# Optimization experiments

Measured on AMD Instinct MI355X. Metric: run time of the kernel, lower is better.

## Reference

```python
import jax, jax.numpy as jnp
import numpy as np

H, R, B, T = 512, 4, 16, 4096

def _glorot(key, shape):
    return jax.random.uniform(key, shape, minval=-1.0, maxval=1.0) * jnp.sqrt(2.0 / sum(shape))

def setup_inputs() -> dict:
    key = jax.random.key(0)
    k1, k2, k3, k4, k5 = jax.random.split(key, 5)
    return {
        "x_seq": jax.random.normal(k5, (B, T, H), dtype=jnp.float32),
        "a_diag": _glorot(k1, (H,)).astype(jnp.float32),
        "p_vec": _glorot(k2, (H, R)).astype(jnp.float32),
        "q_vec": _glorot(k3, (H, R)).astype(jnp.float32),
        "b_mat": _glorot(k4, (H, H)).astype(jnp.float32),
    }

def reference(x_seq, a_diag, p_vec, q_vec, b_mat):
    # A = diag(a_diag) + P Q^T  (DPLR structure, materialized as in the source)
    A = jnp.diag(a_diag) + p_vec @ q_vec.T            # [H, H]
    # Precompute B @ x_t for all timesteps/batches: bx[b,t,k] = sum_h b_mat[k,h] x[b,t,h]
    bx = jnp.einsum("bth,kh->btk", x_seq, b_mat)      # [B, T, H]
    h0 = jnp.zeros((x_seq.shape[0], a_diag.shape[0]), dtype=x_seq.dtype)  # [B, H]

    def step(h, bx_t):
        # h_{t} = A h_{t-1} + B x_t, batched: (h @ A^T)
        h = h @ A.T + bx_t
        return h, h

    _, h_seq = jax.lax.scan(step, h0, jnp.swapaxes(bx, 0, 1))  # [T, B, H]
    return jnp.swapaxes(h_seq, 0, 1)                            # [B, T, H]
```

## Files before the change

kernel.cpp:

```cpp
#include <hip/hip_runtime.h>
#include <hip/hip_bf16.h>

#define H 512
#define RNK 4
#define BATCH 16
#define TT 4096
#define MTOT (BATCH * TT)

#define BM 128
#define BN 128
#define BK 64

#define NCHUNK 128
#define JWARM 32

#define LDK 72

typedef __attribute__((ext_vector_type(8))) short bf16x8;
typedef __attribute__((ext_vector_type(4))) float f32x4;

__device__ inline unsigned short f2bf(float f) {
    unsigned u = __float_as_uint(f);
    u += 0x7FFFu + ((u >> 16) & 1u);
    return (unsigned short)(u >> 16);
}
__device__ inline float bflo(unsigned w) { return __uint_as_float(w << 16); }
__device__ inline float bfhi(unsigned w) { return __uint_as_float(w & 0xFFFF0000u); }
__device__ inline float rfl(float x) {
    return __uint_as_float(__builtin_amdgcn_readfirstlane(__float_as_uint(x)));
}

__global__ __launch_bounds__(256) void convert_kernel(
    const float* __restrict__ src, unsigned short* __restrict__ dst, int n4)
{
    int i = blockIdx.x * blockDim.x + threadIdx.x;
    const int stride = gridDim.x * blockDim.x;
    for (; i < n4; i += stride) {
        float4 v = ((const float4*)src)[i];
        ushort4 o = { f2bf(v.x), f2bf(v.y), f2bf(v.z), f2bf(v.w) };
        ((ushort4*)dst)[i] = o;
    }
}

__global__ __launch_bounds__(256) void gemm_bt_kernel(
    const unsigned short* __restrict__ A,
    const unsigned short* __restrict__ Bm,
    unsigned short* __restrict__ C)
{
    __shared__ unsigned short As[BM * BK];
    __shared__ unsigned short Bs[BN * BK];
    const int tid  = threadIdx.x;
    const int lane = tid & 63;
    const int wave = tid >> 6;
    const int wm = (wave >> 1) * 64;
    const int wn = (wave & 1) * 64;
    const size_t m0 = (size_t)blockIdx.x * BM;
    const int n0 = blockIdx.y * BN;
    const int r  = lane & 15;
    const int qd = lane >> 4;

    f32x4 acc[4][4];
    #pragma unroll
    for (int i = 0; i < 4; ++i)
        #pragma unroll
        for (int j = 0; j < 4; ++j)
            acc[i][j] = (f32x4){0.f, 0.f, 0.f, 0.f};

    for (int k0 = 0; k0 < H; k0 += BK) {
        #pragma unroll
        for (int s = 0; s < 4; ++s) {
            const int seg = wave * 4 + s;
            const int off = seg * 1024 + lane * 16;
            const int row = off >> 7;
            const int inrow = off & 127;
            const char* ga = (const char*)(A + (m0 + row) * H + k0) + inrow;
            const char* gb = (const char*)(Bm + (size_t)(n0 + row) * H + k0) + inrow;
            __builtin_amdgcn_global_load_lds(
                (const __attribute__((address_space(1))) unsigned int*)ga,
                (__attribute__((address_space(3))) unsigned int*)&As[seg * 512], 16, 0, 0);
            __builtin_amdgcn_global_load_lds(
                (const __attribute__((address_space(1))) unsigned int*)gb,
                (__attribute__((address_space(3))) unsigned int*)&Bs[seg * 512], 16, 0, 0);
        }
        __syncthreads();
        #pragma unroll
        for (int kk = 0; kk < BK; kk += 32) {
            bf16x8 af[4], bfr[4];
            #pragma unroll
            for (int i = 0; i < 4; ++i)
                af[i] = *(const bf16x8*)&As[(wm + i * 16 + r) * BK + kk + qd * 8];
            #pragma unroll
            for (int j = 0; j < 4; ++j)
                bfr[j] = *(const bf16x8*)&Bs[(wn + j * 16 + r) * BK + kk + qd * 8];
            #pragma unroll
            for (int i = 0; i < 4; ++i)
                #pragma unroll
                for (int j = 0; j < 4; ++j)
                    acc[i][j] = __builtin_amdgcn_mfma_f32_16x16x32_bf16(
                        af[i], bfr[j], acc[i][j], 0, 0, 0);
        }
        __syncthreads();
    }
    #pragma unroll
    for (int i = 0; i < 4; ++i)
        #pragma unroll
        for (int j = 0; j < 4; ++j)
            #pragma unroll
            for (int e = 0; e < 4; ++e) {
                const size_t m = m0 + wm + i * 16 + qd * 4 + e;
                const int n = n0 + wn + j * 16 + r;
                C[m * H + n] = f2bf(acc[i][j][e]);
            }
}

__global__ __launch_bounds__(64) void scan_bf_kernel(
    const unsigned short* __restrict__ bx, float* __restrict__ out,
    const float* __restrict__ a_diag, const float* __restrict__ p_vec,
    const float* __restrict__ q_vec, int nchunk, int warm_max)
{
    const int lane = threadIdx.x;
    const int c = blockIdx.x;
    const int b = blockIdx.y;
    const int L = TT / nchunk;
    const int d0 = lane * 8;

    float ak[8], g[8];
    float4 pk[8], qk[8];
    #pragma unroll
    for (int j = 0; j < 8; ++j) {
        ak[j] = a_diag[d0 + j];
        pk[j] = *(const float4*)(p_vec + (d0 + j) * RNK);
        qk[j] = *(const float4*)(q_vec + (d0 + j) * RNK);
        g[j] = 0.f;
    }

    float Gx[3][4][4];
    {
        float part[3][16];
        #pragma unroll
        for (int k = 0; k < 3; ++k)
            #pragma unroll
            for (int v = 0; v < 16; ++v) part[k][v] = 0.f;
        #pragma unroll
        for (int d = 0; d < 8; ++d) {
            const float a1 = ak[d], a2 = a1 * a1;
            const float qr[4] = {qk[d].x, qk[d].y, qk[d].z, qk[d].w};
            const float pc[4] = {pk[d].x, pk[d].y, pk[d].z, pk[d].w};
            #pragma unroll
            for (int r = 0; r < 4; ++r)
                #pragma unroll
                for (int cc = 0; cc < 4; ++cc) {
                    const float qp = qr[r] * pc[cc];
                    part[0][r * 4 + cc] += qp;
                    part[1][r * 4 + cc] += qp * a1;
                    part[2][r * 4 + cc] += qp * a2;
                }
        }
        #pragma unroll
        for (int off = 32; off > 0; off >>= 1)
            #pragma unroll
            for (int k = 0; k < 3; ++k)
                #pragma unroll
                for (int v = 0; v < 16; ++v)
                    part[k][v] += __shfl_xor(part[k][v], off);
        #pragma unroll
        for (int k = 0; k < 3; ++k)
            #pragma unroll
            for (int r = 0; r < 4; ++r)
                #pragma unroll
                for (int cc = 0; cc < 4; ++cc)
                    Gx[k][r][cc] = rfl(part[k][r * 4 + cc]);
    }

    const int warm  = (c == 0) ? 0 : warm_max;
    const int steps = warm + L;
    const int nb    = steps >> 2;
    const int tstart = c * L - warm;
    const unsigned short* src = bx + (size_t)b * TT * H + d0;
    float* dst = out + (size_t)b * TT * H + d0;

    uint4 ring[4];
    #pragma unroll
    for (int j = 0; j < 4; ++j)
        ring[j] = *(const uint4*)(src + (size_t)(tstart + j) * H);

    for (int blk = 0; blk < nb; ++blk) {
        const int i0 = blk * 4;
        float yp[4][4];
        float gs[4][8];

        #pragma unroll
        for (int j = 0; j < 4; ++j) {
            float y0 = 0.f, y1 = 0.f, y2 = 0.f, y3 = 0.f;
            #pragma unroll
            for (int d = 0; d < 8; ++d) {
                y0 += qk[d].x * g[d]; y1 += qk[d].y * g[d];
                y2 += qk[d].z * g[d]; y3 += qk[d].w * g[d];
            }
            yp[j][0] = y0; yp[j][1] = y1; yp[j][2] = y2; yp[j][3] = y3;

            const uint4 cur = ring[j];
            int iload = i0 + 4 + j;
            if (iload > steps - 1) iload = steps - 1;
            ring[j] = *(const uint4*)(src + (size_t)(tstart + iload) * H);

            float u[8];
            u[0] = bflo(cur.x); u[1] = bfhi(cur.x);
            u[2] = bflo(cur.y); u[3] = bfhi(cur.y);
            u[4] = bflo(cur.z); u[5] = bfhi(cur.z);
            u[6] = bflo(cur.w); u[7] = bfhi(cur.w);
            #pragma unroll
            for (int d = 0; d < 8; ++d) { g[d] = ak[d] * g[d] + u[d]; gs[j][d] = g[d]; }
        }

        #pragma unroll
        for (int off = 32; off > 0; off >>= 1)
            #pragma unroll
            for (int j = 0; j < 4; ++j)
                #pragma unroll
                for (int r = 0; r < 4; ++r)
                    yp[j][r] += __shfl_xor(yp[j][r], off);

        float sv[4][4];
        #pragma unroll
        for (int r = 0; r < 4; ++r) sv[0][r] = yp[0][r];
        #pragma unroll
        for (int r = 0; r < 4; ++r) {
            float t = yp[1][r];
            #pragma unroll
            for (int cc = 0; cc < 4; ++cc) t += Gx[0][r][cc] * sv[0][cc];
            sv[1][r] = t;
        }
        #pragma unroll
        for (int r = 0; r < 4; ++r) {
            float t = yp[2][r];
            #pragma unroll
            for (int cc = 0; cc < 4; ++cc) t += Gx[1][r][cc] * sv[0][cc];
            #pragma unroll
            for (int cc = 0; cc < 4; ++cc) t += Gx[0][r][cc] * sv[1][cc];
            sv[2][r] = t;
        }
        #pragma unroll
        for (int r = 0; r < 4; ++r) {
            float t = yp[3][r];
            #pragma unroll
            for (int cc = 0; cc < 4; ++cc) t += Gx[2][r][cc] * sv[0][cc];
            #pragma unroll
            for (int cc = 0; cc < 4; ++cc) t += Gx[1][r][cc] * sv[1][cc];
            #pragma unroll
            for (int cc = 0; cc < 4; ++cc) t += Gx[0][r][cc] * sv[2][cc];
            sv[3][r] = t;
        }

        const bool dostore = (i0 >= warm);
        float e[8];
        #pragma unroll
        for (int d = 0; d < 8; ++d) e[d] = 0.f;
        #pragma unroll
        for (int j = 0; j < 4; ++j) {
            #pragma unroll
            for (int d = 0; d < 8; ++d) {
                const float ps = pk[d].x * sv[j][0] + pk[d].y * sv[j][1]
                               + pk[d].z * sv[j][2] + pk[d].w * sv[j][3];
                e[d] = ak[d] * e[d] + ps;
            }
            if (dostore) {
                float* dd = dst + (size_t)(tstart + i0 + j) * H;
                *(float4*)dd       = (float4){gs[j][0] + e[0], gs[j][1] + e[1],
                                              gs[j][2] + e[2], gs[j][3] + e[3]};
                *(float4*)(dd + 4) = (float4){gs[j][4] + e[4], gs[j][5] + e[5],
                                              gs[j][6] + e[6], gs[j][7] + e[7]};
            }
        }
        #pragma unroll
        for (int d = 0; d < 8; ++d) g[d] = gs[3][d] + e[d];
    }
}

__global__ __launch_bounds__(256) void gemm_fused_kernel(
    const float* __restrict__ X, const float* __restrict__ W, float* __restrict__ bx)
{
    __shared__ unsigned short As[BM * LDK];
    __shared__ unsigned short Bs[BN * LDK];
    const int tid  = threadIdx.x;
    const int lane = tid & 63;
    const int wave = tid >> 6;
    const int wm = (wave >> 1) * 64;
    const int wn = (wave & 1) * 64;
    const size_t mbase = (size_t)blockIdx.x * BM;
    const int nbase = blockIdx.y * BN;
    const float* Xb = X + mbase * H;
    const float* Wb = W + (size_t)nbase * H;
    f32x4 acc[4][4];
    #pragma unroll
    for (int i = 0; i < 4; ++i)
        #pragma unroll
        for (int j = 0; j < 4; ++j)
            acc[i][j] = (f32x4){0.f, 0.f, 0.f, 0.f};
    const int r  = lane & 15;
    const int qd = lane >> 4;
    for (int k0 = 0; k0 < H; k0 += BK) {
        #pragma unroll
        for (int i = 0; i < 8; ++i) {
            int idx = tid + i * 256;
            int row = idx >> 4;
            int c4  = (idx & 15) * 4;
            float4 va = *(const float4*)(Xb + (size_t)row * H + k0 + c4);
            float4 vb = *(const float4*)(Wb + (size_t)row * H + k0 + c4);
            ushort4 wa = { f2bf(va.x), f2bf(va.y), f2bf(va.z), f2bf(va.w) };
            ushort4 wb = { f2bf(vb.x), f2bf(vb.y), f2bf(vb.z), f2bf(vb.w) };
            *(ushort4*)&As[row * LDK + c4] = wa;
            *(ushort4*)&Bs[row * LDK + c4] = wb;
        }
        __syncthreads();
        #pragma unroll
        for (int kk = 0; kk < BK; kk += 32) {
            bf16x8 af[4], bfr[4];
            #pragma unroll
            for (int i = 0; i < 4; ++i)
                af[i] = *(const bf16x8*)&As[(wm + i * 16 + r) * LDK + kk + qd * 8];
            #pragma unroll
            for (int j = 0; j < 4; ++j)
                bfr[j] = *(const bf16x8*)&Bs[(wn + j * 16 + r) * LDK + kk + qd * 8];
            #pragma unroll
            for (int i = 0; i < 4; ++i)
                #pragma unroll
                for (int j = 0; j < 4; ++j)
                    acc[i][j] = __builtin_amdgcn_mfma_f32_16x16x32_bf16(
                        af[i], bfr[j], acc[i][j], 0, 0, 0);
        }
        __syncthreads();
    }
    #pragma unroll
    for (int i = 0; i < 4; ++i)
        #pragma unroll
        for (int j = 0; j < 4; ++j)
            #pragma unroll
            for (int e = 0; e < 4; ++e) {
                int m = wm + i * 16 + qd * 4 + e;
                int n = wn + j * 16 + r;
                bx[(mbase + m) * H + nbase + n] = acc[i][j][e];
            }
}

__global__ __launch_bounds__(64) void scan_f32_kernel(
    const float* __restrict__ bx, float* __restrict__ out,
    const float* __restrict__ a_diag, const float* __restrict__ p_vec,
    const float* __restrict__ q_vec)
{
    const int lane = threadIdx.x;
    const int b = blockIdx.y;
    const int d0 = lane * 8;
    float ak[8], hk[8];
    float4 pk[8], qk[8];
    #pragma unroll
    for (int j = 0; j < 8; ++j) {
        ak[j] = a_diag[d0 + j];
        pk[j] = *(const float4*)(p_vec + (d0 + j) * RNK);
        qk[j] = *(const float4*)(q_vec + (d0 + j) * RNK);
        hk[j] = 0.f;
    }
    const float* src = bx + (size_t)b * TT * H + d0;
    float* dst = out + (size_t)b * TT * H + d0;
    for (int i = 0; i < TT; ++i) {
        const float* sp = src + (size_t)i * H;
        float4 va = *(const float4*)sp, vb = *(const float4*)(sp + 4);
        float u[8] = {va.x, va.y, va.z, va.w, vb.x, vb.y, vb.z, vb.w};
        float s0 = 0.f, s1 = 0.f, s2 = 0.f, s3 = 0.f;
        #pragma unroll
        for (int j = 0; j < 8; ++j) {
            s0 += qk[j].x * hk[j]; s1 += qk[j].y * hk[j];
            s2 += qk[j].z * hk[j]; s3 += qk[j].w * hk[j];
        }
        #pragma unroll
        for (int off = 32; off > 0; off >>= 1) {
            s0 += __shfl_xor(s0, off); s1 += __shfl_xor(s1, off);
            s2 += __shfl_xor(s2, off); s3 += __shfl_xor(s3, off);
        }
        #pragma unroll
        for (int j = 0; j < 8; ++j)
            hk[j] = ak[j] * hk[j] + (pk[j].x * s0 + pk[j].y * s1 + pk[j].z * s2 + pk[j].w * s3) + u[j];
        float* d = dst + (size_t)i * H;
        *(float4*)d = (float4){hk[0], hk[1], hk[2], hk[3]};
        *(float4*)(d + 4) = (float4){hk[4], hk[5], hk[6], hk[7]};
    }
}

extern "C" void kernel_launch(void* const* d_in, const int* in_sizes, int n_in,
                              void* d_out, int out_size, void* d_ws, size_t ws_size,
                              hipStream_t stream) {
    (void)in_sizes; (void)n_in; (void)out_size;
    const float* x = (const float*)d_in[0];
    const float* a = (const float*)d_in[1];
    const float* p = (const float*)d_in[2];
    const float* q = (const float*)d_in[3];
    const float* w = (const float*)d_in[4];
    float* out = (float*)d_out;

    const size_t nx    = (size_t)MTOT * H;
    const size_t xbf_b = nx * 2;
    const size_t wbf_b = (size_t)H * H * 2;
    const size_t bxb_b = nx * 2;

    unsigned short *xbf = nullptr, *wbf = nullptr, *bxbf = nullptr;
    if (ws_size >= xbf_b + wbf_b + bxb_b) {
        xbf  = (unsigned short*)d_ws;
        wbf  = xbf + nx;
        bxbf = wbf + (size_t)H * H;
    } else if (ws_size >= bxb_b) {
        xbf  = (unsigned short*)d_out;
        wbf  = xbf + nx;
        bxbf = (unsigned short*)d_ws;
    }

    if (bxbf != nullptr) {
        convert_kernel<<<8192, 256, 0, stream>>>(x, xbf, (int)(nx / 4));
        convert_kernel<<<256, 256, 0, stream>>>(w, wbf, (int)(H * H / 4));
        dim3 g1(MTOT / BM, H / BN), b1(256);
        gemm_bt_kernel<<<g1, b1, 0, stream>>>(xbf, wbf, bxbf);
        dim3 g2(NCHUNK, BATCH), b2(64);
        scan_bf_kernel<<<g2, b2, 0, stream>>>(bxbf, out, a, p, q, NCHUNK, JWARM);
    } else {
        dim3 g1(MTOT / BM, H / BN), b1(256);
        gemm_fused_kernel<<<g1, b1, 0, stream>>>(x, w, out);
        dim3 g2(1, BATCH), b2(64);
        scan_f32_kernel<<<g2, b2, 0, stream>>>(out, out, a, p, q);
    }
}
```

Measured before the change: 342.5 us.

## Fuse fp32-to-bf16 conversion into GEMM loads and remap tile order

Drops the separate conversion kernels for x and W. The GEMM now reads fp32 directly, converts to bf16 in registers, and stores into padded LDS tiles (stride 72) to cut bank conflicts. A 1D grid with a swizzled block-to-tile mapping groups the four N-tiles of each M-block across XCDs. This removes a full write and reread of the bf16 copy of x. In exchange it loses the async global_load_lds path and doubles global read bytes per GEMM tile, since fp32 is read and every M-tile of x is loaded four times.

```diff
diff --git a/kernel.cpp b/kernel.cpp
--- a/kernel.cpp
+++ b/kernel.cpp
@@ -30,57 +30,43 @@
     return __uint_as_float(__builtin_amdgcn_readfirstlane(__float_as_uint(x)));
 }
 
-__global__ __launch_bounds__(256) void convert_kernel(
-    const float* __restrict__ src, unsigned short* __restrict__ dst, int n4)
+__global__ __launch_bounds__(256) void gemm_fused_bt_kernel(
+    const float* __restrict__ X, const float* __restrict__ W, unsigned short* __restrict__ C)
 {
-    int i = blockIdx.x * blockDim.x + threadIdx.x;
-    const int stride = gridDim.x * blockDim.x;
-    for (; i < n4; i += stride) {
-        float4 v = ((const float4*)src)[i];
-        ushort4 o = { f2bf(v.x), f2bf(v.y), f2bf(v.z), f2bf(v.w) };
-        ((ushort4*)dst)[i] = o;
-    }
-}
-
-__global__ __launch_bounds__(256) void gemm_bt_kernel(
-    const unsigned short* __restrict__ A,
-    const unsigned short* __restrict__ Bm,
-    unsigned short* __restrict__ C)
-{
-    __shared__ unsigned short As[BM * BK];
-    __shared__ unsigned short Bs[BN * BK];
+    __shared__ unsigned short As[BM * LDK];
+    __shared__ unsigned short Bs[BN * LDK];
+    const int l = blockIdx.x;
+    const int t = (l & 7) * ((MTOT / BM) * (H / BN) / 8) + (l >> 3);
+    const size_t mbase = (size_t)(t >> 2) * BM;
+    const int nbase = (t & 3) * BN;
+
     const int tid  = threadIdx.x;
     const int lane = tid & 63;
     const int wave = tid >> 6;
     const int wm = (wave >> 1) * 64;
     const int wn = (wave & 1) * 64;
-    const size_t m0 = (size_t)blockIdx.x * BM;
-    const int n0 = blockIdx.y * BN;
+    const float* Xb = X + mbase * H;
+    const float* Wb = W + (size_t)nbase * H;
+    f32x4 acc[4][4];
+    #pragma unroll
+    for (int i = 0; i < 4; ++i)
+        #pragma unroll
+        for (int j = 0; j < 4; ++j)
+            acc[i][j] = (f32x4){0.f, 0.f, 0.f, 0.f};
     const int r  = lane & 15;
     const int qd = lane >> 4;
-
-    f32x4 acc[4][4];
-    #pragma unroll
-    for (int i = 0; i < 4; ++i)
-        #pragma unroll
-        for (int j = 0; j < 4; ++j)
-            acc[i][j] = (f32x4){0.f, 0.f, 0.f, 0.f};
-
     for (int k0 = 0; k0 < H; k0 += BK) {
         #pragma unroll
-        for (int s = 0; s < 4; ++s) {
-            const int seg = wave * 4 + s;
-            const int off = seg * 1024 + lane * 16;
-            const int row = off >> 7;
-            const int inrow = off & 127;
-            const char* ga = (const char*)(A + (m0 + row) * H + k0) + inrow;
-            const char* gb = (const char*)(Bm + (size_t)(n0 + row) * H + k0) + inrow;
-            __builtin_amdgcn_global_load_lds(
-                (const __attribute__((address_space(1))) unsigned int*)ga,
-                (__attribute__((address_space(3))) unsigned int*)&As[seg * 512], 16, 0, 0);
-            __builtin_amdgcn_global_load_lds(
-                (const __attribute__((address_space(1))) unsigned int*)gb,
-                (__attribute__((address_space(3))) unsigned int*)&Bs[seg * 512], 16, 0, 0);
+        for (int i = 0; i < 8; ++i) {
+            int idx = tid + i * 256;
+            int row = idx >> 4;
+            int c4  = (idx & 15) * 4;
+            float4 va = *(const float4*)(Xb + (size_t)row * H + k0 + c4);
+            float4 vb = *(const float4*)(Wb + (size_t)row * H + k0 + c4);
+            ushort4 wa = { f2bf(va.x), f2bf(va.y), f2bf(va.z), f2bf(va.w) };
+            ushort4 wb = { f2bf(vb.x), f2bf(vb.y), f2bf(vb.z), f2bf(vb.w) };
+            *(ushort4*)&As[row * LDK + c4] = wa;
+            *(ushort4*)&Bs[row * LDK + c4] = wb;
         }
         __syncthreads();
         #pragma unroll
@@ -88,10 +74,10 @@
             bf16x8 af[4], bfr[4];
             #pragma unroll
             for (int i = 0; i < 4; ++i)
-                af[i] = *(const bf16x8*)&As[(wm + i * 16 + r) * BK + kk + qd * 8];
+                af[i] = *(const bf16x8*)&As[(wm + i * 16 + r) * LDK + kk + qd * 8];
             #pragma unroll
             for (int j = 0; j < 4; ++j)
-                bfr[j] = *(const bf16x8*)&Bs[(wn + j * 16 + r) * BK + kk + qd * 8];
+                bfr[j] = *(const bf16x8*)&Bs[(wn + j * 16 + r) * LDK + kk + qd * 8];
             #pragma unroll
             for (int i = 0; i < 4; ++i)
                 #pragma unroll
@@ -107,8 +93,8 @@
         for (int j = 0; j < 4; ++j)
             #pragma unroll
             for (int e = 0; e < 4; ++e) {
-                const size_t m = m0 + wm + i * 16 + qd * 4 + e;
-                const int n = n0 + wn + j * 16 + r;
+                const size_t m = mbase + wm + i * 16 + qd * 4 + e;
+                const int n = nbase + wn + j * 16 + r;
                 C[m * H + n] = f2bf(acc[i][j][e]);
             }
 }
@@ -398,26 +384,11 @@
     float* out = (float*)d_out;
 
     const size_t nx    = (size_t)MTOT * H;
-    const size_t xbf_b = nx * 2;
-    const size_t wbf_b = (size_t)H * H * 2;
     const size_t bxb_b = nx * 2;
 
-    unsigned short *xbf = nullptr, *wbf = nullptr, *bxbf = nullptr;
-    if (ws_size >= xbf_b + wbf_b + bxb_b) {
-        xbf  = (unsigned short*)d_ws;
-        wbf  = xbf + nx;
-        bxbf = wbf + (size_t)H * H;
-    } else if (ws_size >= bxb_b) {
-        xbf  = (unsigned short*)d_out;
-        wbf  = xbf + nx;
-        bxbf = (unsigned short*)d_ws;
-    }
-
-    if (bxbf != nullptr) {
-        convert_kernel<<<8192, 256, 0, stream>>>(x, xbf, (int)(nx / 4));
-        convert_kernel<<<256, 256, 0, stream>>>(w, wbf, (int)(H * H / 4));
-        dim3 g1(MTOT / BM, H / BN), b1(256);
-        gemm_bt_kernel<<<g1, b1, 0, stream>>>(xbf, wbf, bxbf);
+    if (d_ws != nullptr && ws_size >= bxb_b) {
+        unsigned short* bxbf = (unsigned short*)d_ws;
+        gemm_fused_bt_kernel<<<(MTOT / BM) * (H / BN), 256, 0, stream>>>(x, w, bxbf);
         dim3 g2(NCHUNK, BATCH), b2(64);
         scan_bf_kernel<<<g2, b2, 0, stream>>>(bxbf, out, a, p, q, NCHUNK, JWARM);
     } else {
```

Result: no change. 347.7 us (+1.5%).

## Fuse fp32-to-bf16 conversion of x into GEMM with register prefetch

Applied to the files above, without the earlier changes.

The separate pass that converts x to bf16 is removed. The GEMM now reads fp32 x directly, converts it in registers and writes padded LDS tiles. The next k-tile of x is prefetched into registers while the MFMAs run, and W is issued via global_load_lds after compute. Block indices are remapped across 8 groups, presumably to improve L2 locality per XCD, and the kernel gets launch bounds of 2 blocks per CU. This removes the write and re-read of a 64 MB bf16 copy of x, at the cost of more VGPRs and doubled fp32 global read bytes inside the GEMM.

```diff
diff --git a/kernel.cpp b/kernel.cpp
--- a/kernel.cpp
+++ b/kernel.cpp
@@ -42,22 +42,26 @@
     }
 }
 
-__global__ __launch_bounds__(256) void gemm_bt_kernel(
-    const unsigned short* __restrict__ A,
-    const unsigned short* __restrict__ Bm,
+__global__ __launch_bounds__(256, 2) void gemm_x32_kernel(
+    const float* __restrict__ X, const unsigned short* __restrict__ Wbf,
     unsigned short* __restrict__ C)
 {
-    __shared__ unsigned short As[BM * BK];
+    __shared__ unsigned short As[BM * LDK];
     __shared__ unsigned short Bs[BN * BK];
+    const int l = blockIdx.x;
+    const int t = (l & 7) * ((MTOT / BM) * (H / BN) / 8) + (l >> 3);
+    const size_t mbase = (size_t)(t >> 2) * BM;
+    const int nbase = (t & 3) * BN;
+
     const int tid  = threadIdx.x;
     const int lane = tid & 63;
     const int wave = tid >> 6;
     const int wm = (wave >> 1) * 64;
     const int wn = (wave & 1) * 64;
-    const size_t m0 = (size_t)blockIdx.x * BM;
-    const int n0 = blockIdx.y * BN;
     const int r  = lane & 15;
     const int qd = lane >> 4;
+    const float* Xb = X + mbase * H;
+    const unsigned short* Wb = Wbf + (size_t)nbase * H;
 
     f32x4 acc[4][4];
     #pragma unroll
@@ -66,29 +70,54 @@
         for (int j = 0; j < 4; ++j)
             acc[i][j] = (f32x4){0.f, 0.f, 0.f, 0.f};
 
-    for (int k0 = 0; k0 < H; k0 += BK) {
+    float4 ra[8];
+    auto loadRA = [&](int kt) {
+        const int k0 = kt * BK;
+        #pragma unroll
+        for (int i = 0; i < 8; ++i) {
+            const int idx = tid + i * 256;
+            const int row = idx >> 4;
+            const int c4  = (idx & 15) * 4;
+            ra[i] = *(const float4*)(Xb + (size_t)row * H + k0 + c4);
+        }
+    };
+    auto issueW = [&](int kt) {
+        const int k0 = kt * BK;
         #pragma unroll
         for (int s = 0; s < 4; ++s) {
             const int seg = wave * 4 + s;
             const int off = seg * 1024 + lane * 16;
             const int row = off >> 7;
             const int inrow = off & 127;
-            const char* ga = (const char*)(A + (m0 + row) * H + k0) + inrow;
-            const char* gb = (const char*)(Bm + (size_t)(n0 + row) * H + k0) + inrow;
-            __builtin_amdgcn_global_load_lds(
-                (const __attribute__((address_space(1))) unsigned int*)ga,
-                (__attribute__((address_space(3))) unsigned int*)&As[seg * 512], 16, 0, 0);
+            const char* gb = (const char*)(Wb + (size_t)row * H + k0) + inrow;
             __builtin_amdgcn_global_load_lds(
                 (const __attribute__((address_space(1))) unsigned int*)gb,
                 (__attribute__((address_space(3))) unsigned int*)&Bs[seg * 512], 16, 0, 0);
         }
+    };
+
+    issueW(0);
+    loadRA(0);
+
+    const int nt = H / BK;
+    for (int kt = 0; kt < nt; ++kt) {
+        #pragma unroll
+        for (int i = 0; i < 8; ++i) {
+            const int idx = tid + i * 256;
+            const int row = idx >> 4;
+            const int c4  = (idx & 15) * 4;
+            const float4 v = ra[i];
+            ushort4 wa = { f2bf(v.x), f2bf(v.y), f2bf(v.z), f2bf(v.w) };
+            *(ushort4*)&As[row * LDK + c4] = wa;
+        }
         __syncthreads();
+        if (kt + 1 < nt) loadRA(kt + 1);
         #pragma unroll
         for (int kk = 0; kk < BK; kk += 32) {
             bf16x8 af[4], bfr[4];
             #pragma unroll
             for (int i = 0; i < 4; ++i)
-                af[i] = *(const bf16x8*)&As[(wm + i * 16 + r) * BK + kk + qd * 8];
+                af[i] = *(const bf16x8*)&As[(wm + i * 16 + r) * LDK + kk + qd * 8];
             #pragma unroll
             for (int j = 0; j < 4; ++j)
                 bfr[j] = *(const bf16x8*)&Bs[(wn + j * 16 + r) * BK + kk + qd * 8];
@@ -100,15 +129,17 @@
                         af[i], bfr[j], acc[i][j], 0, 0, 0);
         }
         __syncthreads();
-    }
+        if (kt + 1 < nt) issueW(kt + 1);
+    }
+
     #pragma unroll
     for (int i = 0; i < 4; ++i)
         #pragma unroll
         for (int j = 0; j < 4; ++j)
             #pragma unroll
             for (int e = 0; e < 4; ++e) {
-                const size_t m = m0 + wm + i * 16 + qd * 4 + e;
-                const int n = n0 + wn + j * 16 + r;
+                const size_t m = mbase + wm + i * 16 + qd * 4 + e;
+                const int n = nbase + wn + j * 16 + r;
                 C[m * H + n] = f2bf(acc[i][j][e]);
             }
 }
@@ -398,26 +429,14 @@
     float* out = (float*)d_out;
 
     const size_t nx    = (size_t)MTOT * H;
-    const size_t xbf_b = nx * 2;
     const size_t wbf_b = (size_t)H * H * 2;
     const size_t bxb_b = nx * 2;
 
-    unsigned short *xbf = nullptr, *wbf = nullptr, *bxbf = nullptr;
-    if (ws_size >= xbf_b + wbf_b + bxb_b) {
-        xbf  = (unsigned short*)d_ws;
-        wbf  = xbf + nx;
-        bxbf = wbf + (size_t)H * H;
-    } else if (ws_size >= bxb_b) {
-        xbf  = (unsigned short*)d_out;
-        wbf  = xbf + nx;
-        bxbf = (unsigned short*)d_ws;
-    }
-
-    if (bxbf != nullptr) {
-        convert_kernel<<<8192, 256, 0, stream>>>(x, xbf, (int)(nx / 4));
+    if (d_ws != nullptr && ws_size >= wbf_b + bxb_b) {
+        unsigned short* wbf  = (unsigned short*)d_ws;
+        unsigned short* bxbf = wbf + (size_t)H * H;
         convert_kernel<<<256, 256, 0, stream>>>(w, wbf, (int)(H * H / 4));
-        dim3 g1(MTOT / BM, H / BN), b1(256);
-        gemm_bt_kernel<<<g1, b1, 0, stream>>>(xbf, wbf, bxbf);
+        gemm_x32_kernel<<<(MTOT / BM) * (H / BN), 256, 0, stream>>>(x, wbf, bxbf);
         dim3 g2(NCHUNK, BATCH), b2(64);
         scan_bf_kernel<<<g2, b2, 0, stream>>>(bxbf, out, a, p, q, NCHUNK, JWARM);
     } else {
```

Result: faster. 313.0 us (-8.6%).
